# Kernel optimization log

Hardware: AMD Instinct MI355X
Metric: run time of the kernel (lower is better)

Reference implementation:

```python
import jax, jax.numpy as jnp
import numpy as np


def _conv1x1(x, w, b):
    # x: [B,C,H,W], w: [Cout,Cin], b: [Cout]  (1x1 conv == per-pixel linear)
    return jnp.einsum('bchw,oc->bohw', x, w) + b[None, :, None, None]


def setup_inputs() -> dict:
    key = jax.random.key(0)
    ks = jax.random.split(key, 8)
    B, C, H, W = 8, 128, 128, 128
    s = 1.0 / np.sqrt(C)
    return {
        'q_feat': jax.random.normal(ks[0], (B, C, H, W), jnp.float32),
        'kv_feat': jax.random.normal(ks[1], (B, C, H, W), jnp.float32),
        'q_w': jax.random.normal(ks[2], (C, C), jnp.float32) * s,
        'q_b': jax.random.normal(ks[3], (C,), jnp.float32) * 0.01,
        'k_w': jax.random.normal(ks[4], (C, C), jnp.float32) * s,
        'k_b': jax.random.normal(ks[5], (C,), jnp.float32) * 0.01,
        'v_w': jax.random.normal(ks[6], (C, C), jnp.float32) * s,
        'v_b': jax.random.normal(ks[7], (C,), jnp.float32) * 0.01,
    }


def reference(q_feat, kv_feat, q_w, q_b, k_w, k_b, v_w, v_b):
    B, C, H, W = q_feat.shape
    q = _conv1x1(q_feat, q_w, q_b).reshape(B, C, H * W)   # [B,C,N]
    k = _conv1x1(kv_feat, k_w, k_b).reshape(B, C, H * W)  # [B,C,N]
    v = _conv1x1(kv_feat, v_w, v_b).reshape(B, C, H * W)  # [B,C,N]
    k_sm = jax.nn.softmax(k, axis=-1)                     # softmax over spatial dim N
    context = jnp.einsum('bcn,bdn->bcd', v, k_sm)         # [B,C,C]
    out = jnp.einsum('bcd,bdn->bcn', context, q)          # [B,C,N]
    return out.reshape(B, C, H, W)
```

## Files before the change

kernel.cpp:

```cpp
#include <hip/hip_runtime.h>
#include <hip/hip_bf16.h>
#include <cstdint>

#define B_ 8
#define C_ 128
#define N_ 16384
#define CHN 512
#define SN 128
#define NST 4
#define NC (N_ / CHN)
#define SN4 64

typedef __attribute__((ext_vector_type(8))) short short8;
typedef __attribute__((ext_vector_type(4))) float f32x4;
typedef __attribute__((ext_vector_type(4))) unsigned short us4;
typedef unsigned short u16;

__device__ __forceinline__ short f2bf(float f) {
  union { float f; unsigned u; } c; c.f = f;
  unsigned r = (c.u + 0x7FFFu + ((c.u >> 16) & 1u)) >> 16;
  return (short)r;
}

__device__ __forceinline__ unsigned cvtpk(float lo, float hi) {
  unsigned r;
  asm("v_cvt_pk_bf16_f32 %0, %1, %2" : "=v"(r) : "v"(lo), "v"(hi));
  return r;
}

union SB { short8 s8; unsigned u[4]; };

__device__ __forceinline__ void gl_lds16(const float* g, float* l) {
  __builtin_amdgcn_global_load_lds(
      (const __attribute__((address_space(1))) void*)g,
      (__attribute__((address_space(3))) void*)l, 16, 0, 0);
}

__device__ __forceinline__ int swz(int row) { return (row ^ (row >> 2)) & 7; }

__global__ __launch_bounds__(256) void k0_wcvt(const float* __restrict__ kw,
                                               const float* __restrict__ vw,
                                               u16* __restrict__ wbf) {
  const int g = blockIdx.x * 256 + threadIdx.x;
  const int mat = g >> 12, o4 = g & 4095;
  const float* src = mat ? vw : kw;
  float4 f = reinterpret_cast<const float4*>(src)[o4];
  us4 s;
  s[0] = (u16)f2bf(f.x); s[1] = (u16)f2bf(f.y);
  s[2] = (u16)f2bf(f.z); s[3] = (u16)f2bf(f.w);
  reinterpret_cast<us4*>(wbf + (size_t)mat * C_ * C_)[o4] = s;
}

#define KA_LOADS(ST_) do {                                                   \
  _Pragma("unroll") for (int h_ = 0; h_ < 2; ++h_)                           \
  _Pragma("unroll") for (int j_ = 0; j_ < 16; ++j_)                          \
    xr[h_][j_] = xw[(size_t)j_ * N_ + (ST_) * SN + h_ * 64 + lane];          \
} while (0)

#define KA_XWRITE(BUF_) do {                                                 \
  _Pragma("unroll") for (int h_ = 0; h_ < 2; ++h_) {                         \
    const int n_ = h_ * 64 + lane;                                           \
    unsigned pk_[8];                                                         \
    _Pragma("unroll") for (int p_ = 0; p_ < 8; ++p_)                         \
      pk_[p_] = cvtpk(xr[h_][2 * p_], xr[h_][2 * p_ + 1]);                   \
    _Pragma("unroll") for (int o_ = 0; o_ < 2; ++o_) {                       \
      uint4 q_;                                                              \
      q_.x = pk_[o_ * 4]; q_.y = pk_[o_ * 4 + 1];                            \
      q_.z = pk_[o_ * 4 + 2]; q_.w = pk_[o_ * 4 + 3];                        \
      *reinterpret_cast<uint4*>(                                             \
          (BUF_) + n_ * SN + ((w * 16 + o_ * 8) ^ ((n_ & 7) << 3))) = q_;    \
    }                                                                        \
  }                                                                          \
} while (0)

__global__ __launch_bounds__(512, 2) void ka_projctx(
    const float* __restrict__ kv, const u16* __restrict__ wbf,
    const float* __restrict__ kb, const float* __restrict__ vb,
    float* __restrict__ part, float* __restrict__ zpart) {
  __shared__ u16 xt[2][C_ * SN];
  __shared__ u16 eks[C_ * SN];
  __shared__ u16 vs [C_ * SN];

  const int b = blockIdx.y, kc = blockIdx.x;
  const int tid = threadIdx.x;
  const int w = tid >> 6, lane = tid & 63;
  const int lg = lane >> 4, li = lane & 15;
  const int mat = w >> 2, dblk = w & 3;
  const int cg = w >> 1, dh = w & 1;

  const float* xb = kv + (size_t)b * C_ * N_ + (size_t)kc * CHN;
  const float* xw = xb + (size_t)(w * 16) * N_;
  const u16* Wm = wbf + (size_t)mat * C_ * C_;
  const float* biasp = mat ? vb : kb;
  u16* S = mat ? vs : eks;

  short8 wreg[2][4];
#pragma unroll
  for (int dt = 0; dt < 2; ++dt)
#pragma unroll
    for (int ks = 0; ks < 4; ++ks)
      wreg[dt][ks] = *reinterpret_cast<const short8*>(
          Wm + (dblk * 32 + dt * 16 + li) * C_ + ks * 32 + lg * 8);
  float bias2[2];
#pragma unroll
  for (int dt = 0; dt < 2; ++dt) bias2[dt] = biasp[dblk * 32 + dt * 16 + li];

  f32x4 acc[2][4] = {};
  float zac[2] = {0.f, 0.f};
  float xr[2][16];

  KA_LOADS(0);
  KA_XWRITE(&xt[0][0]);
  KA_LOADS(1);
  asm volatile("s_waitcnt lgkmcnt(0)" ::: "memory");
  __builtin_amdgcn_s_barrier();
  __builtin_amdgcn_sched_barrier(0);

#pragma unroll
  for (int st = 0; st < NST; ++st) {
    const u16* xc = &xt[st & 1][0];

    if (st < NST - 1) {
      KA_XWRITE(&xt[(st + 1) & 1][0]);
      if (st < NST - 2) KA_LOADS(st + 2);
    }

#pragma unroll
    for (int h2 = 0; h2 < 4; ++h2) {
      f32x4 pacc[2][2] = {};
#pragma unroll
      for (int ntl = 0; ntl < 2; ++ntl) {
        const int n = (h2 * 2 + ntl) * 16 + li;
#pragma unroll
        for (int ks = 0; ks < 4; ++ks) {
          short8 a = *reinterpret_cast<const short8*>(
              xc + n * SN + ((ks * 32 + lg * 8) ^ ((n & 7) << 3)));
#pragma unroll
          for (int dt = 0; dt < 2; ++dt)
            pacc[ntl][dt] = __builtin_amdgcn_mfma_f32_16x16x32_bf16(
                a, wreg[dt][ks], pacc[ntl][dt], 0, 0, 0);
        }
      }
#pragma unroll
      for (int dt = 0; dt < 2; ++dt) {
        const int d = dblk * 32 + dt * 16 + li;
        const float bias = bias2[dt];
#pragma unroll
        for (int ntl = 0; ntl < 2; ++ntl) {
          float v0 = pacc[ntl][dt][0] + bias;
          float v1 = pacc[ntl][dt][1] + bias;
          float v2 = pacc[ntl][dt][2] + bias;
          float v3 = pacc[ntl][dt][3] + bias;
          if (mat == 0) {
            v0 = __expf(v0); v1 = __expf(v1); v2 = __expf(v2); v3 = __expf(v3);
            zac[dt] += (v0 + v1) + (v2 + v3);
          }
          const int nq = (h2 * 2 + ntl) * 16 + lg * 4;
          uint2 pk; pk.x = cvtpk(v0, v1); pk.y = cvtpk(v2, v3);
          *reinterpret_cast<uint2*>(S + d * SN + (nq ^ ((d & 7) << 3))) = pk;
        }
      }
    }
    asm volatile("s_waitcnt lgkmcnt(0)" ::: "memory");
    __builtin_amdgcn_s_barrier();
    __builtin_amdgcn_sched_barrier(0);

#pragma unroll
    for (int kk = 0; kk < 4; ++kk) {
      const int n0 = kk * 32 + lg * 8;
      short8 a[2], bb[4];
#pragma unroll
      for (int am = 0; am < 2; ++am) {
        const int c = cg * 32 + am * 16 + li;
        a[am] = *reinterpret_cast<const short8*>(vs + c * SN + (n0 ^ ((c & 7) << 3)));
      }
#pragma unroll
      for (int dt = 0; dt < 4; ++dt) {
        const int d = dh * 64 + dt * 16 + li;
        bb[dt] = *reinterpret_cast<const short8*>(eks + d * SN + (n0 ^ ((d & 7) << 3)));
      }
#pragma unroll
      for (int am = 0; am < 2; ++am)
#pragma unroll
        for (int dt = 0; dt < 4; ++dt)
          acc[am][dt] = __builtin_amdgcn_mfma_f32_16x16x32_bf16(a[am], bb[dt], acc[am][dt], 0, 0, 0);
    }
    asm volatile("s_waitcnt lgkmcnt(0)" ::: "memory");
    __builtin_amdgcn_s_barrier();
    __builtin_amdgcn_sched_barrier(0);
  }

  float* P = part + ((size_t)kc * B_ + b) * C_ * C_;
#pragma unroll
  for (int am = 0; am < 2; ++am)
#pragma unroll
    for (int dt = 0; dt < 4; ++dt)
#pragma unroll
      for (int r = 0; r < 4; ++r) {
        const int c = cg * 32 + am * 16 + lg * 4 + r;
        const int d = dh * 64 + dt * 16 + li;
        P[c * C_ + d] = acc[am][dt][r];
      }
  if (mat == 0) {
#pragma unroll
    for (int dt = 0; dt < 2; ++dt) {
      float z = zac[dt];
      z += __shfl_xor(z, 16);
      z += __shfl_xor(z, 32);
      if (lg == 0)
        zpart[((size_t)kc * B_ + b) * C_ + dblk * 32 + dt * 16 + li] = z;
    }
  }
}

__global__ __launch_bounds__(128) void kb1_red(const float* __restrict__ part,
                                               float* __restrict__ Psum) {
  const int g = blockIdx.x, b = blockIdx.y, t = threadIdx.x;
  const float4* P4 = reinterpret_cast<const float4*>(part);
  float ax = 0.f, ay = 0.f, az = 0.f, aw = 0.f;
#pragma unroll 4
  for (int kc = 0; kc < NC; ++kc) {
    float4 v = P4[((size_t)kc * B_ + b) * 4096 + g * 128 + t];
    ax += v.x; ay += v.y; az += v.z; aw += v.w;
  }
  float4 o; o.x = ax; o.y = ay; o.z = az; o.w = aw;
  reinterpret_cast<float4*>(Psum)[(size_t)b * 4096 + g * 128 + t] = o;
}

__global__ __launch_bounds__(256) void kb2_fin(
    const float* __restrict__ Psum, const float* __restrict__ zpart,
    const float* __restrict__ qw, const float* __restrict__ qb,
    u16* __restrict__ M, float* __restrict__ T) {
  const int b = blockIdx.y;
  const int cs0 = blockIdx.x * 16;
  const int tid = threadIdx.x;
  __shared__ float cs[16][128];
  __shared__ float Zs[128];
  if (tid < 128) {
    float s = 0.f;
    for (int kc = 0; kc < NC; ++kc)
      s += zpart[((size_t)kc * B_ + b) * C_ + tid];
    Zs[tid] = s;
  }
  __syncthreads();
#pragma unroll
  for (int i = 0; i < 8; ++i) {
    const int e = tid + i * 256;
    const int cl = e >> 7, d = e & 127;
    cs[cl][d] = Psum[((size_t)b * C_ + cs0 + cl) * C_ + d] / Zs[d];
  }
  __syncthreads();
  const int cl = tid >> 4, e0 = (tid & 15) * 8;
  float m[8] = {};
  for (int d = 0; d < 128; ++d) {
    const float cv = cs[cl][d];
    const float* qr = qw + d * C_ + e0;
#pragma unroll
    for (int j = 0; j < 8; ++j) m[j] += cv * qr[j];
  }
  u16* mp = M + ((size_t)b * C_ + cs0 + cl) * C_ + e0;
#pragma unroll
  for (int j = 0; j < 8; ++j) mp[j] = (u16)f2bf(m[j]);
  if (tid < 16) {
    float tv = 0.f;
    for (int d = 0; d < 128; ++d) tv += cs[tid][d] * qb[d];
    T[b * C_ + cs0 + tid] = tv;
  }
}

__global__ __launch_bounds__(256) void k4_out(const u16* __restrict__ M,
                                              const float* __restrict__ T,
                                              const float* __restrict__ q,
                                              float* __restrict__ out) {
  __shared__ float qs[C_ * SN4];
  const int b = blockIdx.y;
  const int n0 = blockIdx.x * 64;
  const int tid = threadIdx.x;
  const int w = tid >> 6, lane = tid & 63;
  const int lg = lane >> 4, li = lane & 15;
  const int r_in = lane >> 4, slot = lane & 15;

  const float* qbp = q + (size_t)b * C_ * N_ + n0;
#pragma unroll
  for (int i = 0; i < 8; ++i) {
    const int row = w * 32 + i * 4 + r_in;
    gl_lds16(qbp + (size_t)row * N_ + 4 * (slot ^ swz(row)), qs + (w * 32 + i * 4) * SN4);
  }

  short8 mreg[2][4];
  const u16* Mb = M + (size_t)b * C_ * C_;
#pragma unroll
  for (int ct = 0; ct < 2; ++ct)
#pragma unroll
    for (int ks = 0; ks < 4; ++ks)
      mreg[ct][ks] = *reinterpret_cast<const short8*>(
          Mb + (w * 32 + ct * 16 + li) * C_ + ks * 32 + lg * 8);
  float tc[2];
#pragma unroll
  for (int ct = 0; ct < 2; ++ct) tc[ct] = T[b * C_ + w * 32 + ct * 16 + li];

  __syncthreads();

  f32x4 acc[2][4] = {};
#pragma unroll
  for (int nt = 0; nt < 4; ++nt) {
    const int n = nt * 16 + li;
#pragma unroll
    for (int ks = 0; ks < 4; ++ks) {
      SB sb;
#pragma unroll
      for (int p = 0; p < 4; ++p) {
        const int d0 = ks * 32 + lg * 8 + 2 * p;
        const float f0 = qs[d0 * SN4 + (n ^ (swz(d0) << 2))];
        const float f1 = qs[(d0 + 1) * SN4 + (n ^ (swz(d0 + 1) << 2))];
        sb.u[p] = cvtpk(f0, f1);
      }
#pragma unroll
      for (int ct = 0; ct < 2; ++ct)
        acc[ct][nt] = __builtin_amdgcn_mfma_f32_16x16x32_bf16(sb.s8, mreg[ct][ks], acc[ct][nt], 0, 0, 0);
    }
  }

#pragma unroll
  for (int ct = 0; ct < 2; ++ct) {
    const int c = w * 32 + ct * 16 + li;
    float* op = out + ((size_t)b * C_ + c) * N_ + n0;
#pragma unroll
    for (int nt = 0; nt < 4; ++nt) {
      float4 v;
      v.x = acc[ct][nt][0] + tc[ct];
      v.y = acc[ct][nt][1] + tc[ct];
      v.z = acc[ct][nt][2] + tc[ct];
      v.w = acc[ct][nt][3] + tc[ct];
      *reinterpret_cast<float4*>(op + nt * 16 + lg * 4) = v;
    }
  }
}

extern "C" void kernel_launch(void* const* d_in, const int* in_sizes, int n_in,
                              void* d_out, int out_size, void* d_ws, size_t ws_size,
                              hipStream_t stream) {
  const float* q_feat  = (const float*)d_in[0];
  const float* kv_feat = (const float*)d_in[1];
  const float* q_w = (const float*)d_in[2];
  const float* q_b = (const float*)d_in[3];
  const float* k_w = (const float*)d_in[4];
  const float* k_b = (const float*)d_in[5];
  const float* v_w = (const float*)d_in[6];
  const float* v_b = (const float*)d_in[7];
  float* out = (float*)d_out;

  char* ws = (char*)d_ws;
  const size_t szPart = (size_t)NC * B_ * C_ * C_ * sizeof(float);
  const size_t szZp   = (size_t)NC * B_ * C_ * sizeof(float);
  const size_t szPs   = (size_t)B_ * C_ * C_ * sizeof(float);
  const size_t szWbf  = (size_t)2 * C_ * C_ * sizeof(u16);
  const size_t szM    = (size_t)B_ * C_ * C_ * sizeof(u16);

  float* part  = (float*)ws;
  float* zpart = (float*)(ws + szPart);
  float* Psum  = (float*)(ws + szPart + szZp);
  u16*   wbf   = (u16*)(ws + szPart + szZp + szPs);
  u16*   M     = (u16*)(ws + szPart + szZp + szPs + szWbf);
  float* T     = (float*)(ws + szPart + szZp + szPs + szWbf + szM);

  k0_wcvt<<<dim3(32), 256, 0, stream>>>(k_w, v_w, wbf);
  ka_projctx<<<dim3(NC, B_), 512, 0, stream>>>(kv_feat, wbf, k_b, v_b, part, zpart);
  kb1_red<<<dim3(32, B_), 128, 0, stream>>>(part, Psum);
  kb2_fin<<<dim3(8, B_), 256, 0, stream>>>(Psum, zpart, q_w, q_b, M, T);
  k4_out<<<dim3(N_ / SN4, B_), 256, 0, stream>>>(M, T, q_feat, out);
}
```

Before: 78.89 us.

## Fold partial-context reduction into finalize kernel and transpose MFMA output stores

Removes the separate kb1_red reduction kernel and the Psum buffer by having kb2_fin sum the per-chunk partial context matrices directly while loading its tile. This saves one launch and one round trip through global memory, at the cost of a serial 32-step loop per element inside a small 64-block grid. The output kernel also swaps the MFMA operand order, so each lane now holds results for four channels at one position. Stores become per-row scalar writes coalesced across lanes instead of float4 writes, with the bias fetched per row.

```diff
diff --git a/kernel.cpp b/kernel.cpp
--- a/kernel.cpp
+++ b/kernel.cpp
@@ -213,22 +213,8 @@
   }
 }
 
-__global__ __launch_bounds__(128) void kb1_red(const float* __restrict__ part,
-                                               float* __restrict__ Psum) {
-  const int g = blockIdx.x, b = blockIdx.y, t = threadIdx.x;
-  const float4* P4 = reinterpret_cast<const float4*>(part);
-  float ax = 0.f, ay = 0.f, az = 0.f, aw = 0.f;
-#pragma unroll 4
-  for (int kc = 0; kc < NC; ++kc) {
-    float4 v = P4[((size_t)kc * B_ + b) * 4096 + g * 128 + t];
-    ax += v.x; ay += v.y; az += v.z; aw += v.w;
-  }
-  float4 o; o.x = ax; o.y = ay; o.z = az; o.w = aw;
-  reinterpret_cast<float4*>(Psum)[(size_t)b * 4096 + g * 128 + t] = o;
-}
-
 __global__ __launch_bounds__(256) void kb2_fin(
-    const float* __restrict__ Psum, const float* __restrict__ zpart,
+    const float* __restrict__ part, const float* __restrict__ zpart,
     const float* __restrict__ qw, const float* __restrict__ qb,
     u16* __restrict__ M, float* __restrict__ T) {
   const int b = blockIdx.y;
@@ -247,7 +233,10 @@
   for (int i = 0; i < 8; ++i) {
     const int e = tid + i * 256;
     const int cl = e >> 7, d = e & 127;
-    cs[cl][d] = Psum[((size_t)b * C_ + cs0 + cl) * C_ + d] / Zs[d];
+    float s = 0.f;
+    for (int kc = 0; kc < NC; ++kc)
+      s += part[(((size_t)kc * B_ + b) * C_ + (cs0 + cl)) * C_ + d];
+    cs[cl][d] = s / Zs[d];
   }
   __syncthreads();
   const int cl = tid >> 4, e0 = (tid & 15) * 8;
@@ -295,9 +284,12 @@
     for (int ks = 0; ks < 4; ++ks)
       mreg[ct][ks] = *reinterpret_cast<const short8*>(
           Mb + (w * 32 + ct * 16 + li) * C_ + ks * 32 + lg * 8);
-  float tc[2];
-#pragma unroll
-  for (int ct = 0; ct < 2; ++ct) tc[ct] = T[b * C_ + w * 32 + ct * 16 + li];
+  float tcv[2][4];
+#pragma unroll
+  for (int ct = 0; ct < 2; ++ct)
+#pragma unroll
+    for (int r = 0; r < 4; ++r)
+      tcv[ct][r] = T[b * C_ + w * 32 + ct * 16 + lg * 4 + r];
 
   __syncthreads();
 
@@ -317,24 +309,21 @@
       }
 #pragma unroll
       for (int ct = 0; ct < 2; ++ct)
-        acc[ct][nt] = __builtin_amdgcn_mfma_f32_16x16x32_bf16(sb.s8, mreg[ct][ks], acc[ct][nt], 0, 0, 0);
-    }
-  }
-
-#pragma unroll
-  for (int ct = 0; ct < 2; ++ct) {
-    const int c = w * 32 + ct * 16 + li;
-    float* op = out + ((size_t)b * C_ + c) * N_ + n0;
-#pragma unroll
-    for (int nt = 0; nt < 4; ++nt) {
-      float4 v;
-      v.x = acc[ct][nt][0] + tc[ct];
-      v.y = acc[ct][nt][1] + tc[ct];
-      v.z = acc[ct][nt][2] + tc[ct];
-      v.w = acc[ct][nt][3] + tc[ct];
-      *reinterpret_cast<float4*>(op + nt * 16 + lg * 4) = v;
-    }
-  }
+        acc[ct][nt] = __builtin_amdgcn_mfma_f32_16x16x32_bf16(mreg[ct][ks], sb.s8, acc[ct][nt], 0, 0, 0);
+    }
+  }
+
+#pragma unroll
+  for (int ct = 0; ct < 2; ++ct)
+#pragma unroll
+    for (int r = 0; r < 4; ++r) {
+      const int c = w * 32 + ct * 16 + lg * 4 + r;
+      float* op = out + ((size_t)b * C_ + c) * N_ + n0;
+      const float t = tcv[ct][r];
+#pragma unroll
+      for (int nt = 0; nt < 4; ++nt)
+        op[nt * 16 + li] = acc[ct][nt][r] + t;
+    }
 }
 
 extern "C" void kernel_launch(void* const* d_in, const int* in_sizes, int n_in,
@@ -353,20 +342,17 @@
   char* ws = (char*)d_ws;
   const size_t szPart = (size_t)NC * B_ * C_ * C_ * sizeof(float);
   const size_t szZp   = (size_t)NC * B_ * C_ * sizeof(float);
-  const size_t szPs   = (size_t)B_ * C_ * C_ * sizeof(float);
   const size_t szWbf  = (size_t)2 * C_ * C_ * sizeof(u16);
   const size_t szM    = (size_t)B_ * C_ * C_ * sizeof(u16);
 
   float* part  = (float*)ws;
   float* zpart = (float*)(ws + szPart);
-  float* Psum  = (float*)(ws + szPart + szZp);
-  u16*   wbf   = (u16*)(ws + szPart + szZp + szPs);
-  u16*   M     = (u16*)(ws + szPart + szZp + szPs + szWbf);
-  float* T     = (float*)(ws + szPart + szZp + szPs + szWbf + szM);
+  u16*   wbf   = (u16*)(ws + szPart + szZp);
+  u16*   M     = (u16*)(ws + szPart + szZp + szWbf);
+  float* T     = (float*)(ws + szPart + szZp + szWbf + szM);
 
   k0_wcvt<<<dim3(32), 256, 0, stream>>>(k_w, v_w, wbf);
   ka_projctx<<<dim3(NC, B_), 512, 0, stream>>>(kv_feat, wbf, k_b, v_b, part, zpart);
-  kb1_red<<<dim3(32, B_), 128, 0, stream>>>(part, Psum);
-  kb2_fin<<<dim3(8, B_), 256, 0, stream>>>(Psum, zpart, q_w, q_b, M, T);
+  kb2_fin<<<dim3(8, B_), 256, 0, stream>>>(part, zpart, q_w, q_b, M, T);
   k4_out<<<dim3(N_ / SN4, B_), 256, 0, stream>>>(M, T, q_feat, out);
 }
```

Measured after the change: 76.22 us. -3.4%, faster.
